# Performance work log

Hardware: AMD Instinct MI355X
Metric: run time of the kernel (lower is better)

Reference implementation:

```python
import jax, jax.numpy as jnp
import numpy as np

B, T, H, D, L = 64, 256, 1024, 1024, 6  # batch, seq_len, hidden, input, num stacked cells


def setup_inputs() -> dict:
    key = jax.random.key(0)
    ks = jax.random.split(key, 8)
    std = 1.0 / H ** 0.5
    u = lambda k, s: jax.random.uniform(k, s, jnp.float32, -std, std)
    return {
        "x": jax.random.normal(ks[0], (B, T, D), jnp.float32),
        "h0": jax.random.normal(ks[1], (L, B, H), jnp.float32),
        "weight_ih": u(ks[2], (H, D)),   # present in module but unused on the h-provided path
        "bias_ih": u(ks[3], (H,)),
        "weight_hh": u(ks[4], (H, H)),
        "bias_bh": u(ks[5], (H,)),
        "w_out": u(ks[6], (1, H)),       # nn.Linear(hidden_size, 1)
        "b_out": u(ks[7], (1,)),
    }


def reference(x, h0, weight_ih, bias_ih, weight_hh, bias_bh, w_out, b_out):
    # Faithful to RNN_Flat.forward with h provided:
    #   for t: for l in 0..5: h[l] = tanh(h[l-1] @ Whh.T + b_ih + h[l] @ Whh.T + b_bh)
    # where for l=0, h[-1] is h[5] carried from the previous time step,
    # and x_t is never consumed on this code path.
    seq_len = x.shape[1]
    Whh_t = weight_hh.T

    def cell(prev, h_l):  # cell_hh: weight_hh used for both projections
        return jnp.tanh(prev @ Whh_t + bias_ih + h_l @ Whh_t + bias_bh)

    def step(h, _):
        prev = h[-1]  # in-place update semantics: layer 0 sees previous step's h[5]
        new = []
        for l in range(L):
            prev = cell(prev, h[l])
            new.append(prev)
        h_new = jnp.stack(new, axis=0)  # [L, B, H]
        return h_new, h_new[-1]

    h_final, top = jax.lax.scan(step, h0, None, length=seq_len)  # top: [T, B, H]
    seq = jnp.swapaxes(top, 0, 1)                                # [B, T, H]
    out = seq @ w_out.T + b_out                                  # [B, T, 1]
    return out, h_final
```

## Files before the change

kernel.cpp:

```cpp
#include <hip/hip_runtime.h>


#define BB 64
#define TT 256
#define HH 1024
#define LL 6
#define NG 8
#define GB 8
#define NQ 32
#define SJ 32
#define NTH 256

#define HSTATE_FLOATS (2ull * BB * LL * HH)
#define FLAGS_OFF   (HSTATE_FLOATS * 4)
#define FLAGS_BYTES ((size_t)NG * NQ * 4)
#define PARTIAL_OFF (FLAGS_OFF + 1024)

__device__ __forceinline__ float2 aload2(const float* p) {
    unsigned long long u = __hip_atomic_load((const unsigned long long*)p,
                                             __ATOMIC_RELAXED, __HIP_MEMORY_SCOPE_AGENT);
    union { unsigned long long u; float2 f; } c; c.u = u; return c.f;
}
__device__ __forceinline__ float aload1(const float* p) {
    return __hip_atomic_load(p, __ATOMIC_RELAXED, __HIP_MEMORY_SCOPE_AGENT);
}
__device__ __forceinline__ void astore1(float* p, float v) {
    __hip_atomic_store(p, v, __ATOMIC_RELAXED, __HIP_MEMORY_SCOPE_AGENT);
}

__global__ void __launch_bounds__(NTH, 1)
rnn_kernel(const float* __restrict__ h0,
           const float* __restrict__ Whh,
           const float* __restrict__ bias_ih,
           const float* __restrict__ bias_bh,
           const float* __restrict__ w_out,
           const float* __restrict__ b_out,
           float* hstate, unsigned* flags, float* partial,
           float* __restrict__ d_out)
{
    __shared__ float4 s4[GB * 256];
    __shared__ float  pred[4][SJ][10];

    const int tid = threadIdx.x;
    const int g   = blockIdx.x & 7;
    const int q   = blockIdx.x >> 3;
    const int gb  = g * GB;
    const int jl  = tid & 31;
    const int ks  = tid >> 5;
    const int wv  = tid >> 6;
    const int jg  = q * SJ + jl;

    float4 wreg[32];
    {
        const float4* wrow = (const float4*)(Whh + (size_t)jg * HH) + ks * 32;
#pragma unroll
        for (int r = 0; r < 32; ++r) wreg[r] = wrow[r];
    }

    const float bias_j = bias_ih[jg] + bias_bh[jg];
    const float wout_j = w_out[jg];
    const float bout   = b_out[0];

    {
        int bb = tid >> 5, k = q * SJ + (tid & 31);
#pragma unroll
        for (int l = 0; l < LL; ++l)
            astore1(&hstate[(((size_t)1 * BB + gb + bb) * LL + l) * HH + k],
                    h0[((size_t)l * BB + gb + bb) * HH + k]);
    }

    unsigned* gflags = flags + g * NQ;
    unsigned barno = 0;

    auto gbar = [&]() {
        ++barno;
        asm volatile("s_waitcnt vmcnt(0)" ::: "memory");
        __syncthreads();
        if (tid == 0)
            __hip_atomic_store(gflags + q, barno, __ATOMIC_RELAXED,
                               __HIP_MEMORY_SCOPE_AGENT);
        if (tid < 64) {
            for (int w = 0; w < 100000; ++w) {
                unsigned v = (tid < NQ)
                    ? __hip_atomic_load(gflags + tid, __ATOMIC_RELAXED,
                                        __HIP_MEMORY_SCOPE_AGENT)
                    : barno;
                if (!~__ballot(v >= barno)) break;
                __builtin_amdgcn_s_sleep(1);
            }
        }
        __syncthreads();
        asm volatile("" ::: "memory");
    };

    gbar();

    for (int t = 0; t < TT; ++t) {
        const int pw = t & 1, pr = pw ^ 1;
        for (int l = 0; l < LL; ++l) {
            const int lp = (l == 0) ? (LL - 1) : (l - 1);
            const int pp = (l == 0) ? pr : pw;

            const float* baseP = hstate + (((size_t)pp * BB + gb) * LL + lp) * HH;
            const float* baseH = hstate + (((size_t)pr * BB + gb) * LL + l ) * HH;
            float2 pa[GB][2], ha[GB][2];
#pragma unroll
            for (int r = 0; r < GB; ++r) {
                const float* P = baseP + (size_t)r * LL * HH + tid * 4;
                const float* H = baseH + (size_t)r * LL * HH + tid * 4;
                pa[r][0] = aload2(P);  pa[r][1] = aload2(P + 2);
                ha[r][0] = aload2(H);  ha[r][1] = aload2(H + 2);
            }
#pragma unroll
            for (int r = 0; r < GB; ++r)
                s4[r * 256 + tid] = make_float4(pa[r][0].x + ha[r][0].x,
                                                pa[r][0].y + ha[r][0].y,
                                                pa[r][1].x + ha[r][1].x,
                                                pa[r][1].y + ha[r][1].y);
            __syncthreads();

            float acc[GB];
#pragma unroll
            for (int b = 0; b < GB; ++b) acc[b] = 0.f;
            const float4* xbase = s4 + ks * 32;
#pragma unroll
            for (int b = 0; b < GB; ++b) {
#pragma unroll
                for (int k4 = 0; k4 < 32; ++k4) {
                    float4 x = xbase[b * 256 + k4];
                    float4 w = wreg[k4];
                    acc[b] = fmaf(w.x, x.x, fmaf(w.y, x.y,
                             fmaf(w.z, x.z, fmaf(w.w, x.w, acc[b]))));
                }
            }

#pragma unroll
            for (int b = 0; b < GB; ++b) acc[b] += __shfl_xor(acc[b], 32);
            if ((tid & 63) < 32) {
#pragma unroll
                for (int b = 0; b < GB; ++b) pred[wv][jl][b] = acc[b];
            }
            __syncthreads();

            const int bb = tid >> 5;
            float ysum = pred[0][jl][bb] + pred[1][jl][bb]
                       + pred[2][jl][bb] + pred[3][jl][bb];
            float y = tanhf(ysum + bias_j);
            astore1(&hstate[(((size_t)pw * BB + gb + bb) * LL + l) * HH + jg], y);

            if (l == LL - 1) {
                float c = y * wout_j;
#pragma unroll
                for (int off = 16; off; off >>= 1) c += __shfl_down(c, off, 32);
                if (jl == 0)
                    astore1(&partial[(size_t)pw * BB * NQ + (size_t)(gb + bb) * NQ + q], c);
            }
            if (t == TT - 1)
                d_out[(size_t)BB * TT + ((size_t)l * BB + gb + bb) * HH + jg] = y;

            gbar();

            if (l == LL - 1 && q == 0 && tid < GB) {
                int bo = gb + tid;
                float s = bout;
#pragma unroll
                for (int qq = 0; qq < NQ; ++qq)
                    s += aload1(&partial[(size_t)pw * BB * NQ + (size_t)bo * NQ + qq]);
                d_out[(size_t)bo * TT + t] = s;
            }
        }
    }
}

extern "C" void kernel_launch(void* const* d_in, const int* in_sizes, int n_in,
                              void* d_out, int out_size, void* d_ws, size_t ws_size,
                              hipStream_t stream) {
    const float* h0      = (const float*)d_in[1];
    const float* bias_ih = (const float*)d_in[3];
    const float* Whh     = (const float*)d_in[4];
    const float* bias_bh = (const float*)d_in[5];
    const float* w_out   = (const float*)d_in[6];
    const float* b_out   = (const float*)d_in[7];

    float*    hstate  = (float*)d_ws;
    unsigned* flags   = (unsigned*)((char*)d_ws + FLAGS_OFF);
    float*    partial = (float*)((char*)d_ws + PARTIAL_OFF);

    hipMemsetAsync(flags, 0, FLAGS_BYTES, stream);
    rnn_kernel<<<NG * NQ, NTH, 0, stream>>>(h0, Whh, bias_ih, bias_bh,
                                            w_out, b_out, hstate, flags, partial,
                                            (float*)d_out);
}
```

Measured before the change: 18.18 ms.

## Prefetch next layer's hidden state early and pad barrier flags to separate lines

The h[l] operand from the previous time step, or h[0] of the current step once layer 5 is reached, is already final before the grid barrier. Its loads are therefore issued right after the shared-memory write for the next layer, overlapping the matvec instead of sitting on the post-barrier critical path. The per-block barrier flags are padded to 128-byte strides so that spinning blocks do not contend on one cache line. The partial-sum layout is regrouped per group so the reducer reads contiguous entries. The spin limit is doubled, and prefetched registers add register pressure.

```diff
diff --git a/kernel.cpp b/kernel.cpp
--- a/kernel.cpp
+++ b/kernel.cpp
@@ -10,11 +10,12 @@
 #define NQ 32
 #define SJ 32
 #define NTH 256
+#define FLAG_PAD 32
 
 #define HSTATE_FLOATS (2ull * BB * LL * HH)
 #define FLAGS_OFF   (HSTATE_FLOATS * 4)
-#define FLAGS_BYTES ((size_t)NG * NQ * 4)
-#define PARTIAL_OFF (FLAGS_OFF + 1024)
+#define FLAGS_BYTES ((size_t)NG * NQ * FLAG_PAD * 4)
+#define PARTIAL_OFF (FLAGS_OFF + FLAGS_BYTES)
 
 __device__ __forceinline__ float2 aload2(const float* p) {
     unsigned long long u = __hip_atomic_load((const unsigned long long*)p,
@@ -69,7 +70,7 @@
                     h0[((size_t)l * BB + gb + bb) * HH + k]);
     }
 
-    unsigned* gflags = flags + g * NQ;
+    unsigned* gflags = flags + (size_t)g * NQ * FLAG_PAD;
     unsigned barno = 0;
 
     auto gbar = [&]() {
@@ -77,13 +78,13 @@
         asm volatile("s_waitcnt vmcnt(0)" ::: "memory");
         __syncthreads();
         if (tid == 0)
-            __hip_atomic_store(gflags + q, barno, __ATOMIC_RELAXED,
-                               __HIP_MEMORY_SCOPE_AGENT);
+            __hip_atomic_store(gflags + (size_t)q * FLAG_PAD, barno,
+                               __ATOMIC_RELAXED, __HIP_MEMORY_SCOPE_AGENT);
         if (tid < 64) {
-            for (int w = 0; w < 100000; ++w) {
+            for (int w = 0; w < 200000; ++w) {
                 unsigned v = (tid < NQ)
-                    ? __hip_atomic_load(gflags + tid, __ATOMIC_RELAXED,
-                                        __HIP_MEMORY_SCOPE_AGENT)
+                    ? __hip_atomic_load(gflags + (size_t)tid * FLAG_PAD,
+                                        __ATOMIC_RELAXED, __HIP_MEMORY_SCOPE_AGENT)
                     : barno;
                 if (!~__ballot(v >= barno)) break;
                 __builtin_amdgcn_s_sleep(1);
@@ -94,6 +95,16 @@
     };
 
     gbar();
+
+    float2 ha[GB][2];
+    {
+        const float* baseH = hstate + (((size_t)1 * BB + gb) * LL + 0) * HH;
+#pragma unroll
+        for (int r = 0; r < GB; ++r) {
+            const float* H = baseH + (size_t)r * LL * HH + tid * 4;
+            ha[r][0] = aload2(H);  ha[r][1] = aload2(H + 2);
+        }
+    }
 
     for (int t = 0; t < TT; ++t) {
         const int pw = t & 1, pr = pw ^ 1;
@@ -102,14 +113,11 @@
             const int pp = (l == 0) ? pr : pw;
 
             const float* baseP = hstate + (((size_t)pp * BB + gb) * LL + lp) * HH;
-            const float* baseH = hstate + (((size_t)pr * BB + gb) * LL + l ) * HH;
-            float2 pa[GB][2], ha[GB][2];
+            float2 pa[GB][2];
 #pragma unroll
             for (int r = 0; r < GB; ++r) {
                 const float* P = baseP + (size_t)r * LL * HH + tid * 4;
-                const float* H = baseH + (size_t)r * LL * HH + tid * 4;
                 pa[r][0] = aload2(P);  pa[r][1] = aload2(P + 2);
-                ha[r][0] = aload2(H);  ha[r][1] = aload2(H + 2);
             }
 #pragma unroll
             for (int r = 0; r < GB; ++r)
@@ -119,6 +127,17 @@
                                                 pa[r][1].y + ha[r][1].y);
             __syncthreads();
 
+            {
+                const int nl  = (l == LL - 1) ? 0  : l + 1;
+                const int npr = (l == LL - 1) ? pw : pr;
+                const float* baseHn = hstate + (((size_t)npr * BB + gb) * LL + nl) * HH;
+#pragma unroll
+                for (int r = 0; r < GB; ++r) {
+                    const float* H = baseHn + (size_t)r * LL * HH + tid * 4;
+                    ha[r][0] = aload2(H);  ha[r][1] = aload2(H + 2);
+                }
+            }
+
             float acc[GB];
 #pragma unroll
             for (int b = 0; b < GB; ++b) acc[b] = 0.f;
@@ -153,7 +172,7 @@
 #pragma unroll
                 for (int off = 16; off; off >>= 1) c += __shfl_down(c, off, 32);
                 if (jl == 0)
-                    astore1(&partial[(size_t)pw * BB * NQ + (size_t)(gb + bb) * NQ + q], c);
+                    astore1(&partial[(((size_t)pw * NG + g) * NQ + q) * GB + bb], c);
             }
             if (t == TT - 1)
                 d_out[(size_t)BB * TT + ((size_t)l * BB + gb + bb) * HH + jg] = y;
@@ -165,7 +184,7 @@
                 float s = bout;
 #pragma unroll
                 for (int qq = 0; qq < NQ; ++qq)
-                    s += aload1(&partial[(size_t)pw * BB * NQ + (size_t)bo * NQ + qq]);
+                    s += aload1(&partial[(((size_t)pw * NG + g) * NQ + qq) * GB + tid]);
                 d_out[(size_t)bo * TT + t] = s;
             }
         }
```

Result: slower. 20.82 ms (+14.5%).

## Replace flag-based group barriers with value-tagged hidden-state polling

Applied to the files above, without the earlier changes.

Drops the per-layer flag barrier. Each stored hidden value now carries an additive tag offset (8/16, or 64 for the initial state) that encodes its time-step parity, so consumers spin on the data itself until the expected tag appears. The output projection moves from a partial-sum buffer with a separate reduction to a per-block dot product against w_out, computed when the next step reads h[5]. This takes a full barrier round trip off the critical path on every layer step. In exchange, the tag offset lowers float precision of the stored state, correctness depends on tag windows never overlapping, and the workspace must be zeroed with a larger memset.

```diff
diff --git a/kernel.cpp b/kernel.cpp
--- a/kernel.cpp
+++ b/kernel.cpp
@@ -10,22 +10,20 @@
 #define NQ 32
 #define SJ 32
 #define NTH 256
-
-#define HSTATE_FLOATS (2ull * BB * LL * HH)
-#define FLAGS_OFF   (HSTATE_FLOATS * 4)
-#define FLAGS_BYTES ((size_t)NG * NQ * 4)
-#define PARTIAL_OFF (FLAGS_OFF + 1024)
-
-__device__ __forceinline__ float2 aload2(const float* p) {
+#define MAXIT (1 << 22)
+
+#define HSTATE_BYTES (2ull * BB * LL * HH * 4)
+
+static __device__ __forceinline__ float2 aload2(const float* p) {
     unsigned long long u = __hip_atomic_load((const unsigned long long*)p,
-                                             __ATOMIC_RELAXED, __HIP_MEMORY_SCOPE_AGENT);
+        __ATOMIC_RELAXED, __HIP_MEMORY_SCOPE_AGENT);
     union { unsigned long long u; float2 f; } c; c.u = u; return c.f;
 }
-__device__ __forceinline__ float aload1(const float* p) {
-    return __hip_atomic_load(p, __ATOMIC_RELAXED, __HIP_MEMORY_SCOPE_AGENT);
-}
-__device__ __forceinline__ void astore1(float* p, float v) {
+static __device__ __forceinline__ void astore1(float* p, float v) {
     __hip_atomic_store(p, v, __ATOMIC_RELAXED, __HIP_MEMORY_SCOPE_AGENT);
+}
+static __device__ __forceinline__ bool ok2(float2 v, float tag, float tol) {
+    return fabsf(v.x - tag) <= tol && fabsf(v.y - tag) <= tol;
 }
 
 __global__ void __launch_bounds__(NTH, 1)
@@ -35,11 +33,12 @@
            const float* __restrict__ bias_bh,
            const float* __restrict__ w_out,
            const float* __restrict__ b_out,
-           float* hstate, unsigned* flags, float* partial,
+           float* hstate,
            float* __restrict__ d_out)
 {
     __shared__ float4 s4[GB * 256];
-    __shared__ float  pred[4][SJ][10];
+    __shared__ float  pred[2][4][SJ][10];
+    __shared__ float  outred[2][4];
 
     const int tid = threadIdx.x;
     const int g   = blockIdx.x & 7;
@@ -57,67 +56,89 @@
         for (int r = 0; r < 32; ++r) wreg[r] = wrow[r];
     }
 
-    const float bias_j = bias_ih[jg] + bias_bh[jg];
-    const float wout_j = w_out[jg];
-    const float bout   = b_out[0];
+    const float  bias_j = bias_ih[jg] + bias_bh[jg];
+    const float  wout_j = w_out[jg];
+    const float4 wo     = ((const float4*)w_out)[tid];
+    const float  bout   = b_out[0];
+    (void)wout_j;
 
     {
         int bb = tid >> 5, k = q * SJ + (tid & 31);
 #pragma unroll
         for (int l = 0; l < LL; ++l)
             astore1(&hstate[(((size_t)1 * BB + gb + bb) * LL + l) * HH + k],
-                    h0[((size_t)l * BB + gb + bb) * HH + k]);
-    }
-
-    unsigned* gflags = flags + g * NQ;
-    unsigned barno = 0;
-
-    auto gbar = [&]() {
-        ++barno;
-        asm volatile("s_waitcnt vmcnt(0)" ::: "memory");
-        __syncthreads();
-        if (tid == 0)
-            __hip_atomic_store(gflags + q, barno, __ATOMIC_RELAXED,
-                               __HIP_MEMORY_SCOPE_AGENT);
-        if (tid < 64) {
-            for (int w = 0; w < 100000; ++w) {
-                unsigned v = (tid < NQ)
-                    ? __hip_atomic_load(gflags + tid, __ATOMIC_RELAXED,
-                                        __HIP_MEMORY_SCOPE_AGENT)
-                    : barno;
-                if (!~__ballot(v >= barno)) break;
+                    h0[((size_t)l * BB + gb + bb) * HH + k] + 64.0f);
+    }
+
+    for (int t = 0; t < TT; ++t) {
+        const int   pw   = t & 1, pr = pw ^ 1;
+        const float tagW = 8.0f + 8.0f * (float)((t >> 1) & 1);
+        const float tagO = 8.0f + 8.0f * (float)(((t - 1) >> 1) & 1);
+        const float tagH = (t == 0) ? 64.0f : tagO;
+        const float tolH = (t == 0) ? 16.0f : 1.0f;
+
+        for (int l = 0; l < LL; ++l) {
+            const int   lp   = (l == 0) ? (LL - 1) : (l - 1);
+            const int   pp   = (l == 0) ? pr : pw;
+            const float tagP = (l == 0) ? tagH : tagW;
+            const float tolP = (l == 0) ? tolH : 1.0f;
+            const int   cp   = l & 1;
+
+            const float* baseP = hstate + (((size_t)pp * BB + gb) * LL + lp) * HH + (tid << 2);
+            const float* baseH = hstate + (((size_t)pr * BB + gb) * LL + l ) * HH + (tid << 2);
+            float2 pa0[GB], pa1[GB], ha0[GB], ha1[GB];
+#pragma unroll
+            for (int r = 0; r < GB; ++r) {
+                const float* P = baseP + (size_t)r * LL * HH;
+                const float* H = baseH + (size_t)r * LL * HH;
+                pa0[r] = aload2(P);  pa1[r] = aload2(P + 2);
+                ha0[r] = aload2(H);  ha1[r] = aload2(H + 2);
+            }
+            unsigned bad = 0;
+#pragma unroll
+            for (int r = 0; r < GB; ++r) {
+                if (!ok2(pa0[r], tagP, tolP)) bad |= 1u << (4 * r);
+                if (!ok2(pa1[r], tagP, tolP)) bad |= 2u << (4 * r);
+                if (!ok2(ha0[r], tagH, tolH)) bad |= 4u << (4 * r);
+                if (!ok2(ha1[r], tagH, tolH)) bad |= 8u << (4 * r);
+            }
+            for (int it = 0; bad && it < MAXIT; ++it) {
                 __builtin_amdgcn_s_sleep(1);
-            }
-        }
-        __syncthreads();
-        asm volatile("" ::: "memory");
-    };
-
-    gbar();
-
-    for (int t = 0; t < TT; ++t) {
-        const int pw = t & 1, pr = pw ^ 1;
-        for (int l = 0; l < LL; ++l) {
-            const int lp = (l == 0) ? (LL - 1) : (l - 1);
-            const int pp = (l == 0) ? pr : pw;
-
-            const float* baseP = hstate + (((size_t)pp * BB + gb) * LL + lp) * HH;
-            const float* baseH = hstate + (((size_t)pr * BB + gb) * LL + l ) * HH;
-            float2 pa[GB][2], ha[GB][2];
-#pragma unroll
-            for (int r = 0; r < GB; ++r) {
-                const float* P = baseP + (size_t)r * LL * HH + tid * 4;
-                const float* H = baseH + (size_t)r * LL * HH + tid * 4;
-                pa[r][0] = aload2(P);  pa[r][1] = aload2(P + 2);
-                ha[r][0] = aload2(H);  ha[r][1] = aload2(H + 2);
-            }
+#pragma unroll
+                for (int r = 0; r < GB; ++r) {
+                    const float* P = baseP + (size_t)r * LL * HH;
+                    const float* H = baseH + (size_t)r * LL * HH;
+                    if (bad & (1u << (4 * r))) { pa0[r] = aload2(P);     if (ok2(pa0[r], tagP, tolP)) bad &= ~(1u << (4 * r)); }
+                    if (bad & (2u << (4 * r))) { pa1[r] = aload2(P + 2); if (ok2(pa1[r], tagP, tolP)) bad &= ~(2u << (4 * r)); }
+                    if (bad & (4u << (4 * r))) { ha0[r] = aload2(H);     if (ok2(ha0[r], tagH, tolH)) bad &= ~(4u << (4 * r)); }
+                    if (bad & (8u << (4 * r))) { ha1[r] = aload2(H + 2); if (ok2(ha1[r], tagH, tolH)) bad &= ~(8u << (4 * r)); }
+                }
+            }
+
 #pragma unroll
             for (int r = 0; r < GB; ++r)
-                s4[r * 256 + tid] = make_float4(pa[r][0].x + ha[r][0].x,
-                                                pa[r][0].y + ha[r][0].y,
-                                                pa[r][1].x + ha[r][1].x,
-                                                pa[r][1].y + ha[r][1].y);
+                s4[r * 256 + tid] = make_float4(
+                    (pa0[r].x - tagP) + (ha0[r].x - tagH),
+                    (pa0[r].y - tagP) + (ha0[r].y - tagH),
+                    (pa1[r].x - tagP) + (ha1[r].x - tagH),
+                    (pa1[r].y - tagP) + (ha1[r].y - tagH));
+
+            if (l == 0 && t > 0 && q < GB) {
+                float val = 0.f;
+#pragma unroll
+                for (int r = 0; r < GB; ++r) if (r == q)
+                    val = (pa0[r].x - tagP) * wo.x + (pa0[r].y - tagP) * wo.y
+                        + (pa1[r].x - tagP) * wo.z + (pa1[r].y - tagP) * wo.w;
+#pragma unroll
+                for (int off = 32; off; off >>= 1) val += __shfl_down(val, off, 64);
+                if ((tid & 63) == 0) outred[t & 1][wv] = val;
+            }
             __syncthreads();
+
+            if (l == 0 && t > 0 && q < GB && tid == 0)
+                d_out[(size_t)(gb + q) * TT + (t - 1)] =
+                    outred[t & 1][0] + outred[t & 1][1] +
+                    outred[t & 1][2] + outred[t & 1][3] + bout;
 
             float acc[GB];
 #pragma unroll
@@ -138,37 +159,38 @@
             for (int b = 0; b < GB; ++b) acc[b] += __shfl_xor(acc[b], 32);
             if ((tid & 63) < 32) {
 #pragma unroll
-                for (int b = 0; b < GB; ++b) pred[wv][jl][b] = acc[b];
+                for (int b = 0; b < GB; ++b) pred[cp][wv][jl][b] = acc[b];
             }
             __syncthreads();
 
             const int bb = tid >> 5;
-            float ysum = pred[0][jl][bb] + pred[1][jl][bb]
-                       + pred[2][jl][bb] + pred[3][jl][bb];
+            float ysum = pred[cp][0][jl][bb] + pred[cp][1][jl][bb]
+                       + pred[cp][2][jl][bb] + pred[cp][3][jl][bb];
             float y = tanhf(ysum + bias_j);
-            astore1(&hstate[(((size_t)pw * BB + gb + bb) * LL + l) * HH + jg], y);
-
-            if (l == LL - 1) {
-                float c = y * wout_j;
-#pragma unroll
-                for (int off = 16; off; off >>= 1) c += __shfl_down(c, off, 32);
-                if (jl == 0)
-                    astore1(&partial[(size_t)pw * BB * NQ + (size_t)(gb + bb) * NQ + q], c);
-            }
+            astore1(&hstate[(((size_t)pw * BB + gb + bb) * LL + l) * HH + jg],
+                    y + tagW);
+
             if (t == TT - 1)
                 d_out[(size_t)BB * TT + ((size_t)l * BB + gb + bb) * HH + jg] = y;
-
-            gbar();
-
-            if (l == LL - 1 && q == 0 && tid < GB) {
-                int bo = gb + tid;
-                float s = bout;
-#pragma unroll
-                for (int qq = 0; qq < NQ; ++qq)
-                    s += aload1(&partial[(size_t)pw * BB * NQ + (size_t)bo * NQ + qq]);
-                d_out[(size_t)bo * TT + t] = s;
-            }
         }
+    }
+
+    if (q < GB) {
+        const float* P = hstate + (((size_t)1 * BB + gb + q) * LL + 5) * HH + (tid << 2);
+        float2 a0 = aload2(P), a1 = aload2(P + 2);
+        for (int it = 0; (!ok2(a0, 16.0f, 1.0f) || !ok2(a1, 16.0f, 1.0f)) && it < MAXIT; ++it) {
+            __builtin_amdgcn_s_sleep(1);
+            a0 = aload2(P);  a1 = aload2(P + 2);
+        }
+        float val = (a0.x - 16.0f) * wo.x + (a0.y - 16.0f) * wo.y
+                  + (a1.x - 16.0f) * wo.z + (a1.y - 16.0f) * wo.w;
+#pragma unroll
+        for (int off = 32; off; off >>= 1) val += __shfl_down(val, off, 64);
+        if ((tid & 63) == 0) outred[0][wv] = val;
+        __syncthreads();
+        if (tid == 0)
+            d_out[(size_t)(gb + q) * TT + (TT - 1)] =
+                outred[0][0] + outred[0][1] + outred[0][2] + outred[0][3] + bout;
     }
 }
 
@@ -182,12 +204,9 @@
     const float* w_out   = (const float*)d_in[6];
     const float* b_out   = (const float*)d_in[7];
 
-    float*    hstate  = (float*)d_ws;
-    unsigned* flags   = (unsigned*)((char*)d_ws + FLAGS_OFF);
-    float*    partial = (float*)((char*)d_ws + PARTIAL_OFF);
-
-    hipMemsetAsync(flags, 0, FLAGS_BYTES, stream);
+    float* hstate = (float*)d_ws;
+
+    hipMemsetAsync(hstate, 0, HSTATE_BYTES, stream);
     rnn_kernel<<<NG * NQ, NTH, 0, stream>>>(h0, Whh, bias_ih, bias_bh,
-                                            w_out, b_out, hstate, flags, partial,
-                                            (float*)d_out);
-}
+                                            w_out, b_out, hstate, (float*)d_out);
+}
```

Result: no change. 18.26 ms (+0.5%).
